# Kernel tuning notes

Hardware: AMD Instinct MI355X
Metric: run time of the kernel (lower is better)

Reference implementation:

```python
import jax, jax.numpy as jnp
import numpy as np

B, S, DIM, H = 2, 4096, 512, 8
HD = DIM // H
SCALE = HD ** -0.5
EPS = 1e-5


def setup_inputs() -> dict:
    key = jax.random.key(0)
    ks = jax.random.split(key, 7)
    std = DIM ** -0.5
    return {
        "x": jax.random.normal(ks[0], (B, S, DIM), dtype=jnp.float32),
        "ln_gamma": jnp.ones((DIM,), jnp.float32),
        "ln_beta": jnp.zeros((DIM,), jnp.float32),
        "w_q": jax.random.normal(ks[1], (DIM, DIM), jnp.float32) * std,
        "w_k": jax.random.normal(ks[2], (DIM, DIM), jnp.float32) * std,
        "w_v": jax.random.normal(ks[3], (DIM, DIM), jnp.float32) * std,
        "w_fc": jax.random.normal(ks[4], (DIM, DIM), jnp.float32) * std,
    }


def reference(x, ln_gamma, ln_beta, w_q, w_k, w_v, w_fc):
    # LayerNorm over last dim
    mu = jnp.mean(x, axis=-1, keepdims=True)
    var = jnp.var(x, axis=-1, keepdims=True)
    xn = (x - mu) * jax.lax.rsqrt(var + EPS) * ln_gamma + ln_beta
    # QKV projections (torch Linear: y = x @ W.T), split into heads -> [B,H,S,HD]
    q = jnp.einsum('bsd,ed->bse', xn, w_q).reshape(B, S, H, HD).transpose(0, 2, 1, 3)
    k = jnp.einsum('bsd,ed->bse', xn, w_k).reshape(B, S, H, HD).transpose(0, 2, 1, 3)
    v = jnp.einsum('bsd,ed->bse', xn, w_v).reshape(B, S, H, HD).transpose(0, 2, 1, 3)
    # scores [B,H,S,S]
    attn = jnp.einsum('bhqd,bhkd->bhqk', q, k) * SCALE
    attn = jax.nn.softmax(attn, axis=-1)
    # dropout is identity in eval mode
    out = jnp.einsum('bhqk,bhkd->bhqd', attn, v)
    out = out.transpose(0, 2, 1, 3).reshape(B, S, DIM)
    return jnp.einsum('bsd,ed->bse', out, w_fc)
```

## Files before the change

### kernel.cpp

```cpp
#include <hip/hip_runtime.h>
#include <cstdint>
#include <cstddef>

typedef unsigned short u16;
typedef unsigned int   u32;
typedef __bf16 bf16x8 __attribute__((ext_vector_type(8)));
typedef float  f32x4  __attribute__((ext_vector_type(4)));
typedef float  f32x16 __attribute__((ext_vector_type(16)));
typedef u16    u16x8  __attribute__((ext_vector_type(8)));
typedef u16    u16x4  __attribute__((ext_vector_type(4)));
typedef u32    u32x2  __attribute__((ext_vector_type(2)));
typedef u32    u32x4  __attribute__((ext_vector_type(4)));

#define DI __device__ __forceinline__

constexpr int SEQ = 4096;
constexpr int DIM = 512;
constexpr int NH  = 8;
constexpr int HD  = 64;
constexpr float ATT_C1 = 0.125f * 1.44269504088896340736f;

DI u16 f2bf(float f) {
  u32 u = __builtin_bit_cast(u32, f);
  u += 0x7fffu + ((u >> 16) & 1u);
  return (u16)(u >> 16);
}

DI u32 pk2(float hi, float lo) {
  u32 uh = __builtin_bit_cast(u32, hi) + 0x8000u;
  u32 ul = __builtin_bit_cast(u32, lo) + 0x8000u;
  return __builtin_amdgcn_perm(uh, ul, 0x07060302u);
}

DI u32 cvtpk(float a, float b) {
  u32 r;
  asm("v_cvt_pk_bf16_f32 %0, %1, %2" : "=v"(r) : "v"(a), "v"(b));
  return r;
}

DI void plswap(u32& a, u32& b) {
  asm("v_permlane32_swap_b32 %0, %1" : "+v"(a), "+v"(b));
}

DI void gl_lds16(const void* g, void* lds) {
  __builtin_amdgcn_global_load_lds(
      (const __attribute__((address_space(1))) void*)g,
      (__attribute__((address_space(3))) void*)lds, 16, 0, 0);
}

__global__ __launch_bounds__(256) void wconv_kernel(
    const float* __restrict__ wq, const float* __restrict__ wk,
    const float* __restrict__ wv, const float* __restrict__ wfc,
    u16* __restrict__ Wb)
{
  const int idx  = blockIdx.x * 256 + threadIdx.x;
  const int base = idx * 8;
  const int mat  = base >> 18;
  const int off  = base & (512 * 512 - 1);
  const float* src = (mat == 0) ? wq : (mat == 1) ? wk : (mat == 2) ? wv : wfc;
  const float4 a = *(const float4*)(src + off);
  const float4 b = *(const float4*)(src + off + 4);
  u32x4 o = { pk2(a.y, a.x), pk2(a.w, a.z), pk2(b.y, b.x), pk2(b.w, b.z) };
  *(u32x4*)(Wb + base) = o;
}

__global__ __launch_bounds__(256) void ln_cast_kernel(
    const float* __restrict__ x, const float* __restrict__ gamma,
    const float* __restrict__ beta, u16* __restrict__ xn)
{
  const int row  = blockIdx.x * 4 + (threadIdx.x >> 6);
  const int lane = threadIdx.x & 63;
  const float* xr = x + (size_t)row * DIM + lane * 8;
  const float4 a = *(const float4*)xr;
  const float4 b = *(const float4*)(xr + 4);
  float s = a.x + a.y + a.z + a.w + b.x + b.y + b.z + b.w;
  float q = a.x*a.x + a.y*a.y + a.z*a.z + a.w*a.w
          + b.x*b.x + b.y*b.y + b.z*b.z + b.w*b.w;
#pragma unroll
  for (int m = 1; m < 64; m <<= 1) {
    s += __shfl_xor(s, m, 64);
    q += __shfl_xor(q, m, 64);
  }
  const float mu = s * (1.0f / DIM);
  const float rs = rsqrtf(q * (1.0f / DIM) - mu * mu + 1e-5f);
  const float4 g0 = *(const float4*)(gamma + lane * 8);
  const float4 g1 = *(const float4*)(gamma + lane * 8 + 4);
  const float4 e0 = *(const float4*)(beta + lane * 8);
  const float4 e1 = *(const float4*)(beta + lane * 8 + 4);
  const float v0 = (a.x - mu) * rs * g0.x + e0.x;
  const float v1 = (a.y - mu) * rs * g0.y + e0.y;
  const float v2 = (a.z - mu) * rs * g0.z + e0.z;
  const float v3 = (a.w - mu) * rs * g0.w + e0.w;
  const float v4 = (b.x - mu) * rs * g1.x + e1.x;
  const float v5 = (b.y - mu) * rs * g1.y + e1.y;
  const float v6 = (b.z - mu) * rs * g1.z + e1.z;
  const float v7 = (b.w - mu) * rs * g1.w + e1.w;
  u32x4 o = { pk2(v1, v0), pk2(v3, v2), pk2(v5, v4), pk2(v7, v6) };
  *(u32x4*)(xn + (size_t)row * DIM + lane * 8) = o;
}

template<int MODE>
__global__ __launch_bounds__(256, 2) void gemm_kernel(
    const u16* __restrict__ A, const u16* __restrict__ Wb,
    u16* __restrict__ Qo, u16* __restrict__ Ko, u16* __restrict__ Vt,
    float* __restrict__ Co)
{
  __shared__ __align__(16) u16 As[128 * 64];
  __shared__ __align__(16) u16 Bs[128 * 64];
  const int m0 = blockIdx.y * 128, n0 = blockIdx.x * 128;
  const int t = threadIdx.x, wave = t >> 6, lane = t & 63;
  const int quad = lane >> 4, l15 = lane & 15;
  const int wm = wave >> 1, wn = wave & 1;
  const u16* Wsrc;
  if (MODE == 0) {
    const int mat = n0 >> 9;
    Wsrc = Wb + (size_t)mat * 512 * 512 + (size_t)(n0 & 511) * DIM;
  } else {
    Wsrc = Wb + (size_t)3 * 512 * 512 + (size_t)n0 * DIM;
  }

  f32x4 acc[4][4];
#pragma unroll
  for (int i = 0; i < 4; i++)
#pragma unroll
    for (int j = 0; j < 4; j++)
#pragma unroll
      for (int r = 0; r < 4; r++) acc[i][j][r] = 0.0f;

  for (int kk = 0; kk < DIM; kk += 64) {
    __syncthreads();
#pragma unroll
    for (int rnd = 0; rnd < 4; rnd++) {
      const int c4 = t + rnd * 256;
      const int r = c4 >> 3, cc = (c4 & 7) * 8;
      const int lbase = (wave + rnd * 4) * 1024;
      gl_lds16(A + (size_t)(m0 + r) * DIM + kk + cc, (char*)As + lbase);
      gl_lds16(Wsrc + (size_t)r * DIM + kk + cc, (char*)Bs + lbase);
    }
    __syncthreads();
#pragma unroll
    for (int kx = 0; kx < 2; kx++) {
      bf16x8 af[4], bfr[4];
#pragma unroll
      for (int i = 0; i < 4; i++)
        af[i] = *(const bf16x8*)&As[(wm * 64 + i * 16 + l15) * 64 +
                                    kx * 32 + quad * 8];
#pragma unroll
      for (int j = 0; j < 4; j++)
        bfr[j] = *(const bf16x8*)&Bs[(wn * 64 + j * 16 + l15) * 64 +
                                     kx * 32 + quad * 8];
#pragma unroll
      for (int i = 0; i < 4; i++)
#pragma unroll
        for (int j = 0; j < 4; j++)
          acc[i][j] = __builtin_amdgcn_mfma_f32_16x16x32_bf16(
              af[i], bfr[j], acc[i][j], 0, 0, 0);
    }
  }

  if (MODE == 1) {
#pragma unroll
    for (int i = 0; i < 4; i++) {
      const int m = m0 + wm * 64 + i * 16 + quad * 4;
#pragma unroll
      for (int j = 0; j < 4; j++) {
        const int n = n0 + wn * 64 + j * 16 + l15;
#pragma unroll
        for (int r = 0; r < 4; r++)
          Co[(size_t)(m + r) * DIM + n] = acc[i][j][r];
      }
    }
  } else {
    const int mat = n0 >> 9;
    const float qs = (mat == 0) ? ATT_C1 : 1.0f;
#pragma unroll
    for (int i = 0; i < 4; i++) {
      const int m = m0 + wm * 64 + i * 16 + quad * 4;
      const int b = m >> 12, s = m & 4095;
#pragma unroll
      for (int j = 0; j < 4; j++) {
        const int ng = (n0 & 511) + wn * 64 + j * 16 + l15;
        const int h = ng >> 6, d = ng & 63;
        if (mat < 2) {
          u16* dst = (mat == 0 ? Qo : Ko) +
                     ((size_t)(b * NH + h) * SEQ) * HD + d;
#pragma unroll
          for (int r = 0; r < 4; r++)
            dst[(size_t)(s + r) * HD] = f2bf(acc[i][j][r] * qs);
        } else {
          u32x2 w;
          w[0] = pk2(acc[i][j][1], acc[i][j][0]);
          w[1] = pk2(acc[i][j][3], acc[i][j][2]);
          *(u32x2*)&Vt[((size_t)(b * NH + h) * HD + d) * SEQ + s] = w;
        }
      }
    }
  }
}

__global__ __launch_bounds__(256, 2) void attn_kernel(
    const u16* __restrict__ Q, const u16* __restrict__ K,
    const u16* __restrict__ Vt, u16* __restrict__ O)
{
  __shared__ __align__(16) char smem[73728];
  const int flat = blockIdx.x + 32 * blockIdx.y;
  const int slot = flat >> 3;
  const int bh = (flat & 7) * 2 + (slot & 1);
  const int qt = slot >> 1;
  const int b = bh >> 3, h = bh & 7;
  const int t = threadIdx.x;
  const int wave = t >> 6, lane = t & 63;
  const int kg = wave >> 1;
  const int qsub = wave & 1;
  const int tg = t & 127;
  const int l31 = lane & 31, hf = lane >> 5;

  const u16* Qb = Q + (size_t)bh * SEQ * HD;
  const u16* Kb = K + (size_t)bh * SEQ * HD;
  const u16* Vb = Vt + (size_t)bh * HD * SEQ;
  const int qw = qt * 128 + qsub * 64;
  const int kc0 = kg * 2048;

  bf16x8 bq[2][4];
#pragma unroll
  for (int qh = 0; qh < 2; qh++)
#pragma unroll
    for (int kk = 0; kk < 4; kk++)
      bq[qh][kk] = *(const bf16x8*)(
          Qb + (size_t)(qw + qh * 32 + l31) * HD + kk * 16 + hf * 8);

  f32x16 oacc[2][2];
#pragma unroll
  for (int qh = 0; qh < 2; qh++)
#pragma unroll
    for (int mt2 = 0; mt2 < 2; mt2++)
#pragma unroll
      for (int r = 0; r < 16; r++) oacc[qh][mt2][r] = 0.0f;
  float lrun0 = 0.0f, lrun1 = 0.0f;

  u16x8 kst[4], vst[4];
#pragma unroll
  for (int it = 0; it < 4; it++) {
    const int c4 = tg + it * 128;
    const int r = c4 >> 3, off = (c4 & 7) * 8;
    kst[it] = *(const u16x8*)(Kb + (size_t)(kc0 + r) * HD + off);
    vst[it] = *(const u16x8*)(Vb + (size_t)r * SEQ + kc0 + off);
  }
  {
    u16 (*K0)[72] = (u16 (*)[72])(smem + kg * 36864);
    u16 (*V0)[72] = (u16 (*)[72])(smem + kg * 36864 + 9216);
#pragma unroll
    for (int it = 0; it < 4; it++) {
      const int c4 = tg + it * 128;
      const int r = c4 >> 3, off = (c4 & 7) * 8;
      *(u16x8*)&K0[r][off] = kst[it];
      *(u16x8*)&V0[r][off] = vst[it];
    }
  }
#pragma unroll
  for (int it = 0; it < 4; it++) {
    const int c4 = tg + it * 128;
    const int r = c4 >> 3, off = (c4 & 7) * 8;
    kst[it] = *(const u16x8*)(Kb + (size_t)(kc0 + 64 + r) * HD + off);
    vst[it] = *(const u16x8*)(Vb + (size_t)r * SEQ + kc0 + 64 + off);
  }
  __syncthreads();

  for (int it2 = 0; it2 < 32; it2++) {
    const int buf = it2 & 1;
    u16 (*Kl)[72] = (u16 (*)[72])(smem + kg * 36864 + buf * 18432);
    u16 (*Vl)[72] = (u16 (*)[72])(smem + kg * 36864 + buf * 18432 + 9216);

#pragma unroll
    for (int mt = 0; mt < 2; mt++) {
      f32x16 s0, s1;
#pragma unroll
      for (int r = 0; r < 16; r++) { s0[r] = 0.0f; s1[r] = 0.0f; }
      __builtin_amdgcn_s_setprio(1);
#pragma unroll
      for (int kk = 0; kk < 4; kk++) {
        const bf16x8 ka =
            *(const bf16x8*)&Kl[mt * 32 + l31][kk * 16 + hf * 8];
        s0 = __builtin_amdgcn_mfma_f32_32x32x16_bf16(ka, bq[0][kk], s0, 0, 0, 0);
        s1 = __builtin_amdgcn_mfma_f32_32x32x16_bf16(ka, bq[1][kk], s1, 0, 0, 0);
      }
      __builtin_amdgcn_s_setprio(0);

#pragma unroll
      for (int r = 0; r < 16; r++) s0[r] = __builtin_amdgcn_exp2f(s0[r]);
      lrun0 += (((s0[0] + s0[1]) + (s0[2] + s0[3])) +
                ((s0[4] + s0[5]) + (s0[6] + s0[7]))) +
               (((s0[8] + s0[9]) + (s0[10] + s0[11])) +
                ((s0[12] + s0[13]) + (s0[14] + s0[15])));
#pragma unroll
      for (int r = 0; r < 16; r++) s1[r] = __builtin_amdgcn_exp2f(s1[r]);
      lrun1 += (((s1[0] + s1[1]) + (s1[2] + s1[3])) +
                ((s1[4] + s1[5]) + (s1[6] + s1[7]))) +
               (((s1[8] + s1[9]) + (s1[10] + s1[11])) +
                ((s1[12] + s1[13]) + (s1[14] + s1[15])));

      u32 a0 = cvtpk(s0[0],  s0[1]),  a1 = cvtpk(s0[2],  s0[3]);
      u32 a2 = cvtpk(s0[4],  s0[5]),  a3 = cvtpk(s0[6],  s0[7]);
      plswap(a0, a2); plswap(a1, a3);
      u32 c0 = cvtpk(s0[8],  s0[9]),  c1 = cvtpk(s0[10], s0[11]);
      u32 c2 = cvtpk(s0[12], s0[13]), c3 = cvtpk(s0[14], s0[15]);
      plswap(c0, c2); plswap(c1, c3);
      u32x4 p00v = { a0, a1, a2, a3 };
      u32x4 p01v = { c0, c1, c2, c3 };
      u32 d0 = cvtpk(s1[0],  s1[1]),  d1 = cvtpk(s1[2],  s1[3]);
      u32 d2 = cvtpk(s1[4],  s1[5]),  d3 = cvtpk(s1[6],  s1[7]);
      plswap(d0, d2); plswap(d1, d3);
      u32 e0 = cvtpk(s1[8],  s1[9]),  e1 = cvtpk(s1[10], s1[11]);
      u32 e2 = cvtpk(s1[12], s1[13]), e3 = cvtpk(s1[14], s1[15]);
      plswap(e0, e2); plswap(e1, e3);
      u32x4 p10v = { d0, d1, d2, d3 };
      u32x4 p11v = { e0, e1, e2, e3 };
      const bf16x8 p00 = __builtin_bit_cast(bf16x8, p00v);
      const bf16x8 p01 = __builtin_bit_cast(bf16x8, p01v);
      const bf16x8 p10 = __builtin_bit_cast(bf16x8, p10v);
      const bf16x8 p11 = __builtin_bit_cast(bf16x8, p11v);

      __builtin_amdgcn_s_setprio(1);
#pragma unroll
      for (int mt2 = 0; mt2 < 2; mt2++) {
        const bf16x8 va0 =
            *(const bf16x8*)&Vl[mt2 * 32 + l31][(mt * 2 + 0) * 16 + hf * 8];
        oacc[0][mt2] = __builtin_amdgcn_mfma_f32_32x32x16_bf16(
            va0, p00, oacc[0][mt2], 0, 0, 0);
        oacc[1][mt2] = __builtin_amdgcn_mfma_f32_32x32x16_bf16(
            va0, p10, oacc[1][mt2], 0, 0, 0);
        const bf16x8 va1 =
            *(const bf16x8*)&Vl[mt2 * 32 + l31][(mt * 2 + 1) * 16 + hf * 8];
        oacc[0][mt2] = __builtin_amdgcn_mfma_f32_32x32x16_bf16(
            va1, p01, oacc[0][mt2], 0, 0, 0);
        oacc[1][mt2] = __builtin_amdgcn_mfma_f32_32x32x16_bf16(
            va1, p11, oacc[1][mt2], 0, 0, 0);
      }
      __builtin_amdgcn_s_setprio(0);
    }

    if (it2 < 31) {
      u16 (*Kn)[72] = (u16 (*)[72])(smem + kg * 36864 + (buf ^ 1) * 18432);
      u16 (*Vn)[72] = (u16 (*)[72])(smem + kg * 36864 + (buf ^ 1) * 18432 + 9216);
#pragma unroll
      for (int it = 0; it < 4; it++) {
        const int c4 = tg + it * 128;
        const int r = c4 >> 3, off = (c4 & 7) * 8;
        *(u16x8*)&Kn[r][off] = kst[it];
        *(u16x8*)&Vn[r][off] = vst[it];
      }
      if (it2 < 30) {
        const int kc2 = kc0 + (it2 + 2) * 64;
#pragma unroll
        for (int it = 0; it < 4; it++) {
          const int c4 = tg + it * 128;
          const int r = c4 >> 3, off = (c4 & 7) * 8;
          kst[it] = *(const u16x8*)(Kb + (size_t)(kc2 + r) * HD + off);
          vst[it] = *(const u16x8*)(Vb + (size_t)r * SEQ + kc2 + off);
        }
      }
    }
    __syncthreads();
  }

  f32x4 (*Rbuf)[2][8][64] = (f32x4 (*)[2][8][64])smem;
  float (*Lbuf)[2][64]    = (float (*)[2][64])(smem + 32768);
  if (kg == 1) {
#pragma unroll
    for (int qh = 0; qh < 2; qh++) {
#pragma unroll
      for (int mt2 = 0; mt2 < 2; mt2++)
#pragma unroll
        for (int gi = 0; gi < 4; gi++) {
          f32x4 w;
#pragma unroll
          for (int r = 0; r < 4; r++) w[r] = oacc[qh][mt2][gi * 4 + r];
          Rbuf[qsub][qh][mt2 * 4 + gi][lane] = w;
        }
      Lbuf[qsub][qh][lane] = (qh == 0) ? lrun0 : lrun1;
    }
  }
  __syncthreads();
  if (kg == 0) {
#pragma unroll
    for (int qh = 0; qh < 2; qh++) {
#pragma unroll
      for (int mt2 = 0; mt2 < 2; mt2++)
#pragma unroll
        for (int gi = 0; gi < 4; gi++) {
          const f32x4 w = Rbuf[qsub][qh][mt2 * 4 + gi][lane];
#pragma unroll
          for (int r = 0; r < 4; r++) oacc[qh][mt2][gi * 4 + r] += w[r];
        }
      float lr = ((qh == 0) ? lrun0 : lrun1) + Lbuf[qsub][qh][lane];
      const float lt = lr + __shfl_xor(lr, 32, 64);
      const float inv = 1.0f / lt;
      const int s = qw + qh * 32 + l31;
      u16* Ob = O + ((size_t)(b * SEQ + s)) * DIM + h * HD;
#pragma unroll
      for (int mt2 = 0; mt2 < 2; mt2++)
#pragma unroll
        for (int g = 0; g < 4; g++) {
          u32x2 w;
          w[0] = pk2(oacc[qh][mt2][g * 4 + 1] * inv,
                     oacc[qh][mt2][g * 4 + 0] * inv);
          w[1] = pk2(oacc[qh][mt2][g * 4 + 3] * inv,
                     oacc[qh][mt2][g * 4 + 2] * inv);
          *(u32x2*)&Ob[mt2 * 32 + g * 8 + hf * 4] = w;
        }
    }
  }
}

extern "C" void kernel_launch(void* const* d_in, const int* in_sizes, int n_in,
                              void* d_out, int out_size, void* d_ws,
                              size_t ws_size, hipStream_t stream)
{
  const float* x     = (const float*)d_in[0];
  const float* gamma = (const float*)d_in[1];
  const float* beta  = (const float*)d_in[2];
  const float* wq    = (const float*)d_in[3];
  const float* wk    = (const float*)d_in[4];
  const float* wv    = (const float*)d_in[5];
  const float* wfc   = (const float*)d_in[6];
  float* out = (float*)d_out;

  char* ws = (char*)d_ws;
  u16* xn = (u16*)(ws);
  u16* Qb = (u16*)(ws + ((size_t)8  << 20));
  u16* Kb = (u16*)(ws + ((size_t)16 << 20));
  u16* Vt = (u16*)(ws + ((size_t)24 << 20));
  u16* Ob = (u16*)(ws + ((size_t)32 << 20));
  u16* Wb = (u16*)(ws + ((size_t)40 << 20));

  wconv_kernel<<<512, 256, 0, stream>>>(wq, wk, wv, wfc, Wb);
  ln_cast_kernel<<<2048, 256, 0, stream>>>(x, gamma, beta, xn);
  gemm_kernel<0><<<dim3(12, 64), 256, 0, stream>>>(xn, Wb, Qb, Kb, Vt, nullptr);
  attn_kernel<<<dim3(32, 16), 256, 0, stream>>>(Qb, Kb, Vt, Ob);
  gemm_kernel<1><<<dim3(4, 64), 256, 0, stream>>>(
      Ob, Wb, nullptr, nullptr, nullptr, out);
}
```

Baseline: 198.3 us.

## Issue K/V prefetch at iteration start and batch both QK^T tiles before softmax

The global prefetch of the next K/V tile moves from the end of each iteration, where it ran two tiles ahead, to the start of the iteration, one tile ahead. The loads now overlap with the current tile's compute within the same iteration. All eight QK^T MFMAs for both 32-row halves are also issued back to back before the exp/PV work, so they form a longer uninterrupted matrix burst. In exchange the prefetch distance shrinks, so load latency is hidden only by one iteration's compute, and four score accumulators are live at once, raising register pressure.

```diff
diff --git a/kernel.cpp b/kernel.cpp
--- a/kernel.cpp
+++ b/kernel.cpp
@@ -257,13 +257,6 @@
       *(u16x8*)&V0[r][off] = vst[it];
     }
   }
-#pragma unroll
-  for (int it = 0; it < 4; it++) {
-    const int c4 = tg + it * 128;
-    const int r = c4 >> 3, off = (c4 & 7) * 8;
-    kst[it] = *(const u16x8*)(Kb + (size_t)(kc0 + 64 + r) * HD + off);
-    vst[it] = *(const u16x8*)(Vb + (size_t)r * SEQ + kc0 + 64 + off);
-  }
   __syncthreads();
 
   for (int it2 = 0; it2 < 32; it2++) {
@@ -271,21 +264,38 @@
     u16 (*Kl)[72] = (u16 (*)[72])(smem + kg * 36864 + buf * 18432);
     u16 (*Vl)[72] = (u16 (*)[72])(smem + kg * 36864 + buf * 18432 + 9216);
 
-#pragma unroll
-    for (int mt = 0; mt < 2; mt++) {
-      f32x16 s0, s1;
-#pragma unroll
-      for (int r = 0; r < 16; r++) { s0[r] = 0.0f; s1[r] = 0.0f; }
-      __builtin_amdgcn_s_setprio(1);
-#pragma unroll
-      for (int kk = 0; kk < 4; kk++) {
-        const bf16x8 ka =
-            *(const bf16x8*)&Kl[mt * 32 + l31][kk * 16 + hf * 8];
-        s0 = __builtin_amdgcn_mfma_f32_32x32x16_bf16(ka, bq[0][kk], s0, 0, 0, 0);
-        s1 = __builtin_amdgcn_mfma_f32_32x32x16_bf16(ka, bq[1][kk], s1, 0, 0, 0);
+    if (it2 < 31) {
+      const int kc2 = kc0 + (it2 + 1) * 64;
+#pragma unroll
+      for (int it = 0; it < 4; it++) {
+        const int c4 = tg + it * 128;
+        const int r = c4 >> 3, off = (c4 & 7) * 8;
+        kst[it] = *(const u16x8*)(Kb + (size_t)(kc2 + r) * HD + off);
+        vst[it] = *(const u16x8*)(Vb + (size_t)r * SEQ + kc2 + off);
       }
-      __builtin_amdgcn_s_setprio(0);
-
+    }
+
+    f32x16 sA0, sA1, sB0, sB1;
+#pragma unroll
+    for (int r = 0; r < 16; r++) {
+      sA0[r] = 0.0f; sA1[r] = 0.0f; sB0[r] = 0.0f; sB1[r] = 0.0f;
+    }
+    __builtin_amdgcn_s_setprio(1);
+#pragma unroll
+    for (int kk = 0; kk < 4; kk++) {
+      const bf16x8 ka = *(const bf16x8*)&Kl[l31][kk * 16 + hf * 8];
+      sA0 = __builtin_amdgcn_mfma_f32_32x32x16_bf16(ka, bq[0][kk], sA0, 0, 0, 0);
+      sA1 = __builtin_amdgcn_mfma_f32_32x32x16_bf16(ka, bq[1][kk], sA1, 0, 0, 0);
+    }
+#pragma unroll
+    for (int kk = 0; kk < 4; kk++) {
+      const bf16x8 kb = *(const bf16x8*)&Kl[32 + l31][kk * 16 + hf * 8];
+      sB0 = __builtin_amdgcn_mfma_f32_32x32x16_bf16(kb, bq[0][kk], sB0, 0, 0, 0);
+      sB1 = __builtin_amdgcn_mfma_f32_32x32x16_bf16(kb, bq[1][kk], sB1, 0, 0, 0);
+    }
+    __builtin_amdgcn_s_setprio(0);
+
+    auto smpv = [&](f32x16 s0, f32x16 s1, int sl) {
 #pragma unroll
       for (int r = 0; r < 16; r++) s0[r] = __builtin_amdgcn_exp2f(s0[r]);
       lrun0 += (((s0[0] + s0[1]) + (s0[2] + s0[3])) +
@@ -324,20 +334,22 @@
 #pragma unroll
       for (int mt2 = 0; mt2 < 2; mt2++) {
         const bf16x8 va0 =
-            *(const bf16x8*)&Vl[mt2 * 32 + l31][(mt * 2 + 0) * 16 + hf * 8];
+            *(const bf16x8*)&Vl[mt2 * 32 + l31][(sl + 0) * 16 + hf * 8];
         oacc[0][mt2] = __builtin_amdgcn_mfma_f32_32x32x16_bf16(
             va0, p00, oacc[0][mt2], 0, 0, 0);
         oacc[1][mt2] = __builtin_amdgcn_mfma_f32_32x32x16_bf16(
             va0, p10, oacc[1][mt2], 0, 0, 0);
         const bf16x8 va1 =
-            *(const bf16x8*)&Vl[mt2 * 32 + l31][(mt * 2 + 1) * 16 + hf * 8];
+            *(const bf16x8*)&Vl[mt2 * 32 + l31][(sl + 1) * 16 + hf * 8];
         oacc[0][mt2] = __builtin_amdgcn_mfma_f32_32x32x16_bf16(
             va1, p01, oacc[0][mt2], 0, 0, 0);
         oacc[1][mt2] = __builtin_amdgcn_mfma_f32_32x32x16_bf16(
             va1, p11, oacc[1][mt2], 0, 0, 0);
       }
       __builtin_amdgcn_s_setprio(0);
-    }
+    };
+    smpv(sA0, sA1, 0);
+    smpv(sB0, sB1, 2);
 
     if (it2 < 31) {
       u16 (*Kn)[72] = (u16 (*)[72])(smem + kg * 36864 + (buf ^ 1) * 18432);
@@ -348,16 +360,6 @@
         const int r = c4 >> 3, off = (c4 & 7) * 8;
         *(u16x8*)&Kn[r][off] = kst[it];
         *(u16x8*)&Vn[r][off] = vst[it];
-      }
-      if (it2 < 30) {
-        const int kc2 = kc0 + (it2 + 2) * 64;
-#pragma unroll
-        for (int it = 0; it < 4; it++) {
-          const int c4 = tg + it * 128;
-          const int r = c4 >> 3, off = (c4 & 7) * 8;
-          kst[it] = *(const u16x8*)(Kb + (size_t)(kc2 + r) * HD + off);
-          vst[it] = *(const u16x8*)(Vb + (size_t)r * SEQ + kc2 + off);
-        }
       }
     }
     __syncthreads();
```

After: 197.4 us. About the same (-0.4%).

## Double-buffer GEMM tiles via register prefetch with padded LDS rows

Applied to the files above, without the earlier changes.

Replaces the direct global-to-LDS loads in the projection GEMM with register-staged loads into a double-buffered LDS tile, prefetching the next K-slice while MFMAs run on the current one. LDS rows are padded to 72 elements to reduce bank conflicts on the fragment reads. Each K step now needs one barrier instead of two. In exchange it uses more VGPRs for the staging registers and doubles the LDS footprint, which may reduce occupancy at the 2-blocks-per-CU launch bound.

```diff
diff --git a/kernel.cpp b/kernel.cpp
--- a/kernel.cpp
+++ b/kernel.cpp
@@ -40,12 +40,6 @@
 
 DI void plswap(u32& a, u32& b) {
   asm("v_permlane32_swap_b32 %0, %1" : "+v"(a), "+v"(b));
-}
-
-DI void gl_lds16(const void* g, void* lds) {
-  __builtin_amdgcn_global_load_lds(
-      (const __attribute__((address_space(1))) void*)g,
-      (__attribute__((address_space(3))) void*)lds, 16, 0, 0);
 }
 
 __global__ __launch_bounds__(256) void wconv_kernel(
@@ -105,8 +99,8 @@
     u16* __restrict__ Qo, u16* __restrict__ Ko, u16* __restrict__ Vt,
     float* __restrict__ Co)
 {
-  __shared__ __align__(16) u16 As[128 * 64];
-  __shared__ __align__(16) u16 Bs[128 * 64];
+  __shared__ u16 As[2][128][72];
+  __shared__ u16 Bs[2][128][72];
   const int m0 = blockIdx.y * 128, n0 = blockIdx.x * 128;
   const int t = threadIdx.x, wave = t >> 6, lane = t & 63;
   const int quad = lane >> 4, l15 = lane & 15;
@@ -127,28 +121,44 @@
 #pragma unroll
       for (int r = 0; r < 4; r++) acc[i][j][r] = 0.0f;
 
-  for (int kk = 0; kk < DIM; kk += 64) {
-    __syncthreads();
-#pragma unroll
-    for (int rnd = 0; rnd < 4; rnd++) {
-      const int c4 = t + rnd * 256;
-      const int r = c4 >> 3, cc = (c4 & 7) * 8;
-      const int lbase = (wave + rnd * 4) * 1024;
-      gl_lds16(A + (size_t)(m0 + r) * DIM + kk + cc, (char*)As + lbase);
-      gl_lds16(Wsrc + (size_t)r * DIM + kk + cc, (char*)Bs + lbase);
-    }
-    __syncthreads();
+  u16x8 av[4], bv[4];
+#pragma unroll
+  for (int it = 0; it < 4; it++) {
+    const int c4 = t + it * 256;
+    const int r = c4 >> 3, cc = (c4 & 7) * 8;
+    av[it] = *(const u16x8*)(A + (size_t)(m0 + r) * DIM + cc);
+    bv[it] = *(const u16x8*)(Wsrc + (size_t)r * DIM + cc);
+  }
+#pragma unroll
+  for (int it = 0; it < 4; it++) {
+    const int c4 = t + it * 256;
+    const int r = c4 >> 3, cc = (c4 & 7) * 8;
+    *(u16x8*)&As[0][r][cc] = av[it];
+    *(u16x8*)&Bs[0][r][cc] = bv[it];
+  }
+  __syncthreads();
+
+  for (int ks = 0; ks < 8; ks++) {
+    const int cur = ks & 1;
+    if (ks < 7) {
+      const int kk = (ks + 1) * 64;
+#pragma unroll
+      for (int it = 0; it < 4; it++) {
+        const int c4 = t + it * 256;
+        const int r = c4 >> 3, cc = (c4 & 7) * 8;
+        av[it] = *(const u16x8*)(A + (size_t)(m0 + r) * DIM + kk + cc);
+        bv[it] = *(const u16x8*)(Wsrc + (size_t)r * DIM + kk + cc);
+      }
+    }
 #pragma unroll
     for (int kx = 0; kx < 2; kx++) {
       bf16x8 af[4], bfr[4];
 #pragma unroll
       for (int i = 0; i < 4; i++)
-        af[i] = *(const bf16x8*)&As[(wm * 64 + i * 16 + l15) * 64 +
-                                    kx * 32 + quad * 8];
+        af[i] = *(const bf16x8*)&As[cur][wm * 64 + i * 16 + l15][kx * 32 + quad * 8];
 #pragma unroll
       for (int j = 0; j < 4; j++)
-        bfr[j] = *(const bf16x8*)&Bs[(wn * 64 + j * 16 + l15) * 64 +
-                                     kx * 32 + quad * 8];
+        bfr[j] = *(const bf16x8*)&Bs[cur][wn * 64 + j * 16 + l15][kx * 32 + quad * 8];
 #pragma unroll
       for (int i = 0; i < 4; i++)
 #pragma unroll
@@ -156,6 +166,16 @@
           acc[i][j] = __builtin_amdgcn_mfma_f32_16x16x32_bf16(
               af[i], bfr[j], acc[i][j], 0, 0, 0);
     }
+    if (ks < 7) {
+#pragma unroll
+      for (int it = 0; it < 4; it++) {
+        const int c4 = t + it * 256;
+        const int r = c4 >> 3, cc = (c4 & 7) * 8;
+        *(u16x8*)&As[cur ^ 1][r][cc] = av[it];
+        *(u16x8*)&Bs[cur ^ 1][r][cc] = bv[it];
+      }
+    }
+    __syncthreads();
   }
 
   if (MODE == 1) {
```

New measurement: 194.3 us. -2.0%, faster.
